# Kernel optimization log

Hardware: AMD Instinct MI355X
Metric: run time of the kernel (lower is better)

## Reference

```python
import jax, jax.numpy as jnp
import numpy as np


def setup_inputs() -> dict:
    key = jax.random.key(0)
    k1, k2 = jax.random.split(key)
    B, N = 16, 131072
    x = jax.random.normal(k1, (B, N, 3), dtype=jnp.float32)
    farthest_init = jax.random.randint(k2, (B,), 0, N)  # torch.randint(0, N, (B,))
    return {"x": x, "farthest_init": farthest_init, "npoint": 4096}


def reference(x, farthest_init, npoint):
    """Farthest point sampling: returns sampled point indices [B, npoint].

    npoint corresponds to keypoint_num = int(max(density * volume)) in the
    original module; it is shape-determining so it is passed as a static int.
    """
    xyz = x[:, :, :3]                      # [B, N, 3]
    B, N, _ = xyz.shape
    INF = jnp.float32(1e10)                # matches torch's 1e10 init distance

    def step(carry, _):
        distance, farthest = carry         # [B, N], [B]
        # gather current centroid per batch: xyz[b, farthest[b], :]
        centroid = jnp.take_along_axis(xyz, farthest[:, None, None], axis=1)  # [B,1,3]
        dist = jnp.sum((xyz - centroid) ** 2, axis=-1)  # [B, N]
        distance = jnp.minimum(distance, dist)          # masked update dist<distance
        new_farthest = jnp.argmax(distance, axis=-1)    # [B]
        return (distance, new_farthest), farthest       # emit index chosen this step

    init = (jnp.full((B, N), INF, dtype=xyz.dtype), farthest_init)
    _, centroids = jax.lax.scan(step, init, None, length=npoint)  # [npoint, B]
    return centroids.T                                            # [B, npoint]
```

## Files before the change

### kernel.cpp

```cpp
#include <hip/hip_runtime.h>
#include <stdint.h>

#define NBATCH 16
#define NPTS   131072
#define NPOINT 4096
#define KWG    16
#define TPB    1024
#define NWAVE  (TPB/64)
#define PPT    (NPTS/(KWG*TPB))
#define SEG    (NPTS/KWG)

typedef unsigned long long u64;
typedef unsigned int u32;

__device__ __forceinline__ u64 shfl_xor_u64(u64 v, int m) {
    u32 lo=(u32)v, hi=(u32)(v>>32);
    lo=(u32)__shfl_xor((int)lo,m,64);
    hi=(u32)__shfl_xor((int)hi,m,64);
    return ((u64)hi<<32)|lo;
}
__device__ __forceinline__ u64 shfl_u64(u64 v, int s) {
    u32 lo=(u32)v, hi=(u32)(v>>32);
    lo=(u32)__shfl((int)lo,s,64);
    hi=(u32)__shfl((int)hi,s,64);
    return ((u64)hi<<32)|lo;
}

__global__ __launch_bounds__(TPB, 4) void fps_kernel(
    const float* __restrict__ xyz, const int* __restrict__ finit,
    int* __restrict__ out, u64* __restrict__ ring)
{
    const int b    = blockIdx.x >> 4;
    const int w    = blockIdx.x & 15;
    const int tid  = threadIdx.x;
    const int lane = tid & 63;
    const int wv   = tid >> 6;

    const float* xb = xyz + (size_t)b*NPTS*3;
    const int base = w * SEG;

    float px[PPT], py[PPT], pz[PPT], pd[PPT];
    u32 inv[PPT];
    #pragma unroll
    for (int j = 0; j < PPT; ++j) {
        int idx = base + j*TPB + tid;
        px[j] = xb[(size_t)idx*3+0];
        py[j] = xb[(size_t)idx*3+1];
        pz[j] = xb[(size_t)idx*3+2];
        pd[j] = 1e10f;
        inv[j] = (u32)(NPTS-1-idx);
    }

    __shared__ u64   lds_keys[NWAVE];
    __shared__ float bc[3];

    const int f0 = finit[b];
    if (w == 0 && tid == 0) out[b*NPOINT] = f0;
    float cx = xb[(size_t)f0*3+0];
    float cy = xb[(size_t)f0*3+1];
    float cz = xb[(size_t)f0*3+2];

    u64* bring = ring + (size_t)b * 2 * KWG;

    for (int t = 1; t < NPOINT; ++t) {
        float mx = -1.0f;
        #pragma unroll
        for (int j = 0; j < PPT; ++j) {
            float dx = __fsub_rn(px[j], cx);
            float dy = __fsub_rn(py[j], cy);
            float dz = __fsub_rn(pz[j], cz);
            float d  = __fmaf_rn(dz, dz, __fmaf_rn(dy, dy, __fmul_rn(dx, dx)));
            float nd = fminf(pd[j], d);
            pd[j] = nd;
            mx = fmaxf(mx, nd);
        }
        u32 binv = 0;
        #pragma unroll
        for (int j = 0; j < PPT; ++j) {
            u32 cand = (inv[j] > binv) ? inv[j] : binv;
            binv = (pd[j] == mx) ? cand : binv;
        }
        float mxw = mx;
        #pragma unroll
        for (int m = 1; m < 64; m <<= 1)
            mxw = fmaxf(mxw, __uint_as_float((u32)__shfl_xor((int)__float_as_uint(mxw), m, 64)));
        u32 bv = (mx == mxw) ? binv : 0u;
        #pragma unroll
        for (int m = 1; m < 64; m <<= 1) {
            u32 o = (u32)__shfl_xor((int)bv, m, 64);
            bv = (o > bv) ? o : bv;
        }
        if (lane == 0)
            lds_keys[wv] = ((u64)__float_as_uint(mxw) << 17) | (u64)bv;
        __syncthreads();

        const int p = t & 1;
        if (wv == 0) {
            const u64 tt = (u64)(u32)t;
            const u64 tg = tt << 49;
            u64 kb = lds_keys[lane & 15];
            #pragma unroll
            for (int m = 1; m < 16; m <<= 1) {
                u64 o = shfl_xor_u64(kb, m);
                kb = (o > kb) ? o : kb;
            }
            u64* bp = bring + (p << 4);
            if (lane == 0)
                __hip_atomic_store(&bp[w], tg | kb, __ATOMIC_RELAXED,
                                   __HIP_MEMORY_SCOPE_AGENT);
            u64 g = tg | kb;
            float sxl = 0.f, syl = 0.f, szl = 0.f;
            if (lane < 16) {
                if (lane != w) {
                    u64* sp = &bp[lane];
                    u64 ga = __hip_atomic_load(sp, __ATOMIC_RELAXED, __HIP_MEMORY_SCOPE_AGENT);
                    for (;;) {
                        u64 gb = __hip_atomic_load(sp, __ATOMIC_RELAXED, __HIP_MEMORY_SCOPE_AGENT);
                        if ((ga >> 49) == tt) { g = ga; break; }
                        ga = __hip_atomic_load(sp, __ATOMIC_RELAXED, __HIP_MEMORY_SCOPE_AGENT);
                        if ((gb >> 49) == tt) { g = gb; break; }
                    }
                }
                int bi_l = (NPTS-1) - (int)(g & 0x1FFFF);
                sxl = xb[(size_t)bi_l*3+0];
                syl = xb[(size_t)bi_l*3+1];
                szl = xb[(size_t)bi_l*3+2];
            }
            u64 k2 = (lane < 16) ? g : 0;
            int P = lane & 15;
            #pragma unroll
            for (int m = 1; m < 16; m <<= 1) {
                u64 o  = shfl_xor_u64(k2, m);
                int oP = __shfl_xor(P, m, 64);
                if (o > k2) { k2 = o; P = oP; }
            }
            int Pstar = __shfl(P, 0, 64);
            u64 Kstar = shfl_u64(k2, 0);
            int bi = (NPTS-1) - (int)(Kstar & 0x1FFFF);
            float cxn = __shfl(sxl, Pstar, 64);
            float cyn = __shfl(syl, Pstar, 64);
            float czn = __shfl(szl, Pstar, 64);
            if (lane == 0) {
                bc[0] = cxn; bc[1] = cyn; bc[2] = czn;
                if (w == 0) out[b*NPOINT + t] = bi;
            }
        }
        __syncthreads();
        cx = bc[0]; cy = bc[1]; cz = bc[2];
    }
}

extern "C" void kernel_launch(void* const* d_in, const int* in_sizes, int n_in,
                              void* d_out, int out_size, void* d_ws, size_t ws_size,
                              hipStream_t stream) {
    const float* xyz   = (const float*)d_in[0];
    const int*   finit = (const int*)d_in[1];
    int*         out   = (int*)d_out;
    u64*         ring  = (u64*)d_ws;

    void* args[] = { (void*)&xyz, (void*)&finit, (void*)&out, (void*)&ring };
    dim3 grid(NBATCH * KWG), block(TPB);
    if (hipLaunchCooperativeKernel((const void*)fps_kernel, grid, block, args, 0, stream)
        != hipSuccess) {
        fps_kernel<<<grid, block, 0, stream>>>(xyz, finit, out, ring);
    }
}
```

Measured before the change: 9.490 ms.

## Halve block size and replace shuffle reductions with DPP-based wave reductions

Block size drops from 1024 to 512 threads, so each thread holds twice as many points and the per-block barrier and LDS reduction span 8 waves instead of 16. Wave-level max reductions switch from ds_bpermute shuffles to DPP row ops plus swizzle, and the float max is reduced as unsigned bits. The per-thread max and argmax loops now use four independent accumulators to shorten dependency chains. The winning segment is derived from the index by shift instead of a tracked lane id. Costs are higher register pressure from the larger per-thread point count and lower occupancy from launch bounds of 2.

```diff
diff --git a/kernel.cpp b/kernel.cpp
--- a/kernel.cpp
+++ b/kernel.cpp
@@ -5,28 +5,46 @@
 #define NPTS   131072
 #define NPOINT 4096
 #define KWG    16
-#define TPB    1024
+#define TPB    512
 #define NWAVE  (TPB/64)
 #define PPT    (NPTS/(KWG*TPB))
 #define SEG    (NPTS/KWG)
+#define SEGSH  13
 
 typedef unsigned long long u64;
 typedef unsigned int u32;
 
-__device__ __forceinline__ u64 shfl_xor_u64(u64 v, int m) {
-    u32 lo=(u32)v, hi=(u32)(v>>32);
-    lo=(u32)__shfl_xor((int)lo,m,64);
-    hi=(u32)__shfl_xor((int)hi,m,64);
-    return ((u64)hi<<32)|lo;
+template<int CTRL>
+__device__ __forceinline__ u32 dpp32(u32 x) {
+    return (u32)__builtin_amdgcn_update_dpp(0, (int)x, CTRL, 0xf, 0xf, true);
 }
-__device__ __forceinline__ u64 shfl_u64(u64 v, int s) {
-    u32 lo=(u32)v, hi=(u32)(v>>32);
-    lo=(u32)__shfl((int)lo,s,64);
-    hi=(u32)__shfl((int)hi,s,64);
-    return ((u64)hi<<32)|lo;
+__device__ __forceinline__ u32 umax_(u32 a, u32 b) { return a > b ? a : b; }
+
+template<int CTRL>
+__device__ __forceinline__ u64 dpp64max(u64 x) {
+    u32 lo = dpp32<CTRL>((u32)x);
+    u32 hi = dpp32<CTRL>((u32)(x >> 32));
+    u64 o = ((u64)hi << 32) | lo;
+    return o > x ? o : x;
+}
+__device__ __forceinline__ u32 wave_umax(u32 x) {
+    x = umax_(x, dpp32<0xB1>(x));
+    x = umax_(x, dpp32<0x4E>(x));
+    x = umax_(x, dpp32<0x124>(x));
+    x = umax_(x, dpp32<0x128>(x));
+    x = umax_(x, (u32)__builtin_amdgcn_ds_swizzle((int)x, 0x401F));
+    x = umax_(x, (u32)__shfl_xor((int)x, 32, 64));
+    return x;
+}
+__device__ __forceinline__ u64 row16_umax64(u64 k) {
+    k = dpp64max<0xB1>(k);
+    k = dpp64max<0x4E>(k);
+    k = dpp64max<0x124>(k);
+    k = dpp64max<0x128>(k);
+    return k;
 }
 
-__global__ __launch_bounds__(TPB, 4) void fps_kernel(
+__global__ __launch_bounds__(TPB, 2) void fps_kernel(
     const float* __restrict__ xyz, const int* __restrict__ finit,
     int* __restrict__ out, u64* __restrict__ ring)
 {
@@ -36,34 +54,34 @@
     const int lane = tid & 63;
     const int wv   = tid >> 6;
 
-    const float* xb = xyz + (size_t)b*NPTS*3;
+    const float* xb = xyz + (size_t)b * NPTS * 3;
     const int base = w * SEG;
 
     float px[PPT], py[PPT], pz[PPT], pd[PPT];
     u32 inv[PPT];
     #pragma unroll
     for (int j = 0; j < PPT; ++j) {
-        int idx = base + j*TPB + tid;
-        px[j] = xb[(size_t)idx*3+0];
-        py[j] = xb[(size_t)idx*3+1];
-        pz[j] = xb[(size_t)idx*3+2];
+        int idx = base + j * TPB + tid;
+        px[j] = xb[(size_t)idx * 3 + 0];
+        py[j] = xb[(size_t)idx * 3 + 1];
+        pz[j] = xb[(size_t)idx * 3 + 2];
         pd[j] = 1e10f;
-        inv[j] = (u32)(NPTS-1-idx);
+        inv[j] = (u32)(NPTS - 1 - idx);
     }
 
     __shared__ u64   lds_keys[NWAVE];
     __shared__ float bc[3];
 
     const int f0 = finit[b];
-    if (w == 0 && tid == 0) out[b*NPOINT] = f0;
-    float cx = xb[(size_t)f0*3+0];
-    float cy = xb[(size_t)f0*3+1];
-    float cz = xb[(size_t)f0*3+2];
+    if (w == 0 && tid == 0) out[b * NPOINT] = f0;
+    float cx = xb[(size_t)f0 * 3 + 0];
+    float cy = xb[(size_t)f0 * 3 + 1];
+    float cz = xb[(size_t)f0 * 3 + 2];
 
-    u64* bring = ring + (size_t)b * 2 * KWG;
+    u64* bp = ring + (size_t)b * 2 * KWG;
 
     for (int t = 1; t < NPOINT; ++t) {
-        float mx = -1.0f;
+        float m0 = -1.0f, m1 = -1.0f, m2 = -1.0f, m3 = -1.0f;
         #pragma unroll
         for (int j = 0; j < PPT; ++j) {
             float dx = __fsub_rn(px[j], cx);
@@ -72,77 +90,66 @@
             float d  = __fmaf_rn(dz, dz, __fmaf_rn(dy, dy, __fmul_rn(dx, dx)));
             float nd = fminf(pd[j], d);
             pd[j] = nd;
-            mx = fmaxf(mx, nd);
+            if ((j & 3) == 0)      m0 = fmaxf(m0, nd);
+            else if ((j & 3) == 1) m1 = fmaxf(m1, nd);
+            else if ((j & 3) == 2) m2 = fmaxf(m2, nd);
+            else                   m3 = fmaxf(m3, nd);
         }
-        u32 binv = 0;
+        float mx = fmaxf(fmaxf(m0, m1), fmaxf(m2, m3));
+        u32 mxb = wave_umax(__float_as_uint(mx));
+        u32 b0 = 0, b1 = 0, b2 = 0, b3 = 0;
         #pragma unroll
         for (int j = 0; j < PPT; ++j) {
-            u32 cand = (inv[j] > binv) ? inv[j] : binv;
-            binv = (pd[j] == mx) ? cand : binv;
+            bool tie = (__float_as_uint(pd[j]) == mxb);
+            if ((j & 3) == 0)      b0 = tie ? umax_(b0, inv[j]) : b0;
+            else if ((j & 3) == 1) b1 = tie ? umax_(b1, inv[j]) : b1;
+            else if ((j & 3) == 2) b2 = tie ? umax_(b2, inv[j]) : b2;
+            else                   b3 = tie ? umax_(b3, inv[j]) : b3;
         }
-        float mxw = mx;
-        #pragma unroll
-        for (int m = 1; m < 64; m <<= 1)
-            mxw = fmaxf(mxw, __uint_as_float((u32)__shfl_xor((int)__float_as_uint(mxw), m, 64)));
-        u32 bv = (mx == mxw) ? binv : 0u;
-        #pragma unroll
-        for (int m = 1; m < 64; m <<= 1) {
-            u32 o = (u32)__shfl_xor((int)bv, m, 64);
-            bv = (o > bv) ? o : bv;
-        }
+        u32 bv = wave_umax(umax_(umax_(b0, b1), umax_(b2, b3)));
         if (lane == 0)
-            lds_keys[wv] = ((u64)__float_as_uint(mxw) << 17) | (u64)bv;
+            lds_keys[wv] = ((u64)mxb << 17) | (u64)bv;
         __syncthreads();
 
         const int p = t & 1;
         if (wv == 0) {
             const u64 tt = (u64)(u32)t;
             const u64 tg = tt << 49;
-            u64 kb = lds_keys[lane & 15];
-            #pragma unroll
-            for (int m = 1; m < 16; m <<= 1) {
-                u64 o = shfl_xor_u64(kb, m);
-                kb = (o > kb) ? o : kb;
-            }
-            u64* bp = bring + (p << 4);
+            u64 kb = lds_keys[lane & (NWAVE - 1)];
+            kb = row16_umax64(kb);
+            u64* bpp = bp + (p << 4);
             if (lane == 0)
-                __hip_atomic_store(&bp[w], tg | kb, __ATOMIC_RELAXED,
+                __hip_atomic_store(&bpp[w], tg | kb, __ATOMIC_RELAXED,
                                    __HIP_MEMORY_SCOPE_AGENT);
             u64 g = tg | kb;
+            if (lane < 16 && lane != w) {
+                u64* sp = &bpp[lane];
+                u64 ga = __hip_atomic_load(sp, __ATOMIC_RELAXED, __HIP_MEMORY_SCOPE_AGENT);
+                for (;;) {
+                    u64 gb = __hip_atomic_load(sp, __ATOMIC_RELAXED, __HIP_MEMORY_SCOPE_AGENT);
+                    if ((ga >> 49) == tt) { g = ga; break; }
+                    ga = __hip_atomic_load(sp, __ATOMIC_RELAXED, __HIP_MEMORY_SCOPE_AGENT);
+                    if ((gb >> 49) == tt) { g = gb; break; }
+                }
+            }
             float sxl = 0.f, syl = 0.f, szl = 0.f;
             if (lane < 16) {
-                if (lane != w) {
-                    u64* sp = &bp[lane];
-                    u64 ga = __hip_atomic_load(sp, __ATOMIC_RELAXED, __HIP_MEMORY_SCOPE_AGENT);
-                    for (;;) {
-                        u64 gb = __hip_atomic_load(sp, __ATOMIC_RELAXED, __HIP_MEMORY_SCOPE_AGENT);
-                        if ((ga >> 49) == tt) { g = ga; break; }
-                        ga = __hip_atomic_load(sp, __ATOMIC_RELAXED, __HIP_MEMORY_SCOPE_AGENT);
-                        if ((gb >> 49) == tt) { g = gb; break; }
-                    }
+                int bi_l = (NPTS - 1) - (int)(g & 0x1FFFF);
+                sxl = xb[(size_t)bi_l * 3 + 0];
+                syl = xb[(size_t)bi_l * 3 + 1];
+                szl = xb[(size_t)bi_l * 3 + 2];
+            }
+            u64 K = row16_umax64((lane < 16) ? g : 0);
+            if (lane < 16) {
+                int bi    = (NPTS - 1) - (int)(K & 0x1FFFF);
+                int Pstar = bi >> SEGSH;
+                float cxn = __shfl(sxl, Pstar, 64);
+                float cyn = __shfl(syl, Pstar, 64);
+                float czn = __shfl(szl, Pstar, 64);
+                if (lane == 0) {
+                    bc[0] = cxn; bc[1] = cyn; bc[2] = czn;
+                    if (w == 0) out[b * NPOINT + t] = bi;
                 }
-                int bi_l = (NPTS-1) - (int)(g & 0x1FFFF);
-                sxl = xb[(size_t)bi_l*3+0];
-                syl = xb[(size_t)bi_l*3+1];
-                szl = xb[(size_t)bi_l*3+2];
-            }
-            u64 k2 = (lane < 16) ? g : 0;
-            int P = lane & 15;
-            #pragma unroll
-            for (int m = 1; m < 16; m <<= 1) {
-                u64 o  = shfl_xor_u64(k2, m);
-                int oP = __shfl_xor(P, m, 64);
-                if (o > k2) { k2 = o; P = oP; }
-            }
-            int Pstar = __shfl(P, 0, 64);
-            u64 Kstar = shfl_u64(k2, 0);
-            int bi = (NPTS-1) - (int)(Kstar & 0x1FFFF);
-            float cxn = __shfl(sxl, Pstar, 64);
-            float cyn = __shfl(syl, Pstar, 64);
-            float czn = __shfl(szl, Pstar, 64);
-            if (lane == 0) {
-                bc[0] = cxn; bc[1] = cyn; bc[2] = czn;
-                if (w == 0) out[b*NPOINT + t] = bi;
             }
         }
         __syncthreads();
```

After: 7.814 ms. 1.21x faster.
